# Optimization experiments

Measured on AMD Instinct MI355X. Metric: run time of the kernel, lower is better.

## Reference

```python
import jax, jax.numpy as jnp
import numpy as np
from itertools import permutations

NB_OBJ = 5
DIM_BODY = 10
DIM_OBJ = 15


def _lin(k, fi, fo):
    lim = 1.0 / np.sqrt(fi)
    k1, k2 = jax.random.split(k)
    w = jax.random.uniform(k1, (fi, fo), jnp.float32, -lim, lim)
    b = jax.random.uniform(k2, (fo,), jnp.float32, -lim, lim)
    return w, b


def setup_inputs() -> dict:
    key = jax.random.key(0)
    ks = jax.random.split(key, 12)
    B = 16384
    d = {}
    d["obs"] = jax.random.normal(ks[0], (B, DIM_BODY + NB_OBJ * DIM_OBJ), jnp.float32)
    d["act"] = jax.random.normal(ks[1], (B, 4), jnp.float32)
    d["ag"] = jax.random.uniform(ks[2], (B, 30), dtype=jnp.float32)
    d["g"] = jax.random.uniform(ks[3], (B, 30), dtype=jnp.float32)
    # GnnMessagePassing: Linear(46 -> 128), relu
    d["mp_w"], d["mp_b"] = _lin(ks[4], 46, 128)
    # PhiCriticDeepSet: two parallel 2-layer MLPs (157 -> 256 -> 256), relu
    d["phi_w1"], d["phi_b1"] = _lin(ks[5], 157, 256)
    d["phi_w2"], d["phi_b2"] = _lin(ks[6], 256, 256)
    d["phi_w3"], d["phi_b3"] = _lin(ks[7], 157, 256)
    d["phi_w4"], d["phi_b4"] = _lin(ks[8], 256, 256)
    # RhoCriticDeepSet: two Linear(256 -> 1)
    d["rho_w1"], d["rho_b1"] = _lin(ks[9], 256, 1)
    d["rho_w2"], d["rho_b2"] = _lin(ks[10], 256, 1)
    edges = np.array(list(permutations(range(NB_OBJ), 2)), np.int32)  # [20, 2]
    d["edges_src"] = jnp.array(edges[:, 0])
    d["edges_dst"] = jnp.array(edges[:, 1])
    d["pred_ids"] = jnp.array([[i, (i + 10) % 30] for i in range(20)], jnp.int32)  # [20, 2]
    inc = [[j for j in range(20) if edges[j, 1] == i] for i in range(NB_OBJ)]
    d["incoming"] = jnp.array(inc, jnp.int32)  # [5, 4]
    return d


def reference(obs, act, ag, g, mp_w, mp_b, phi_w1, phi_b1, phi_w2, phi_b2,
              phi_w3, phi_b3, phi_w4, phi_b4, rho_w1, rho_b1, rho_w2, rho_b2,
              edges_src, edges_dst, pred_ids, incoming):
    B = obs.shape[0]
    E = edges_src.shape[0]
    obs_body = obs[:, :DIM_BODY]                                   # [B, 10]
    obs_obj = obs[:, DIM_BODY:].reshape(B, NB_OBJ, DIM_OBJ)        # [B, 5, 15]
    # --- message passing over the 20 directed edges ---
    delta_g = g - ag
    dg_sel = delta_g[:, pred_ids]                                  # [B, E, 2]
    src = obs_obj[:, edges_src, :]                                 # [B, E, 15]
    dst = obs_obj[:, edges_dst, :]                                 # [B, E, 15]
    base = jnp.concatenate([obs_body, act], axis=-1)               # [B, 14]
    base_e = jnp.broadcast_to(base[:, None, :], (B, E, base.shape[-1]))
    inp_mp = jnp.concatenate([base_e, dg_sel, src, dst], axis=-1)  # [B, E, 46]
    edge_feat = jax.nn.relu(jnp.einsum('bef,fo->beo', inp_mp, mp_w) + mp_b)  # [B, E, 128]
    # --- segment-sum of incoming edges per object ---
    agg = edge_feat[:, incoming, :].sum(axis=2)                    # [B, 5, 128]
    ba = jnp.concatenate([act, obs_body], axis=-1)                 # [B, 14]
    ba_n = jnp.broadcast_to(ba[:, None, :], (B, NB_OBJ, ba.shape[-1]))
    inp = jnp.concatenate([ba_n, obs_obj, agg], axis=-1)           # [B, 5, 157]
    # --- phi deep-set critics ---
    h1 = jax.nn.relu(jnp.einsum('bnf,fh->bnh', inp, phi_w1) + phi_b1)
    o1 = jax.nn.relu(h1 @ phi_w2 + phi_b2).sum(axis=1)             # [B, 256]
    h2 = jax.nn.relu(jnp.einsum('bnf,fh->bnh', inp, phi_w3) + phi_b3)
    o2 = jax.nn.relu(h2 @ phi_w4 + phi_b4).sum(axis=1)             # [B, 256]
    # --- rho heads ---
    q1 = o1 @ rho_w1 + rho_b1                                      # [B, 1]
    q2 = o2 @ rho_w2 + rho_b2                                      # [B, 1]
    return q1, q2
```

## Files before the change

kernel.cpp:

```cpp
#include <hip/hip_runtime.h>
#include <hip/hip_bf16.h>

typedef __bf16 bf16x8 __attribute__((ext_vector_type(8)));
typedef __bf16 bf16x4 __attribute__((ext_vector_type(4)));
typedef float f32x4 __attribute__((ext_vector_type(4)));

#define MFMA(a, b, c) __builtin_amdgcn_mfma_f32_16x16x32_bf16(a, b, c, 0, 0, 0)

constexpr int MP_OFF = 0;
constexpr int W1_OFF = 8192;
constexpr int W2_OFF = 49152;
constexpr int W3_OFF = 114688;
constexpr int W4_OFF = 155648;
constexpr int WS_TOTAL = 221184;
constexpr size_t WS_BYTES = (size_t)WS_TOTAL * 2;

__device__ __forceinline__ float ldf(const void* p, int i, bool f32) {
    return f32 ? ((const float*)p)[i] : (float)(((const __bf16*)p)[i]);
}
__device__ __forceinline__ int geti(const int* p, int i, bool i64) {
    return p[i64 ? 2 * i : i];
}

__global__ void swz(const void* __restrict__ mp, const void* __restrict__ w1,
                    const void* __restrict__ w2, const void* __restrict__ w3,
                    const void* __restrict__ w4, __bf16* __restrict__ ws,
                    const unsigned short* __restrict__ uo, int* __restrict__ flags) {
    __shared__ int s_fw, s_fi;
    int tid = threadIdx.x;
    if (tid == 0) { s_fw = 0; s_fi = 0; }
    __syncthreads();
    const unsigned short* uw = (const unsigned short*)w2;
    int d = 0;
    for (int i = tid; i < 8192; i += 256)
        d |= (((uw[i] >> 7) & 0xFF) == 0xFF) ? 1 : 0;
    if (d) atomicOr(&s_fw, 1);
    if (blockIdx.x == 0) {
        int d0 = 0;
        for (int i = tid; i < 8192; i += 256)
            d0 |= (((uo[i] >> 7) & 0xFF) == 0xFF) ? 1 : 0;
        if (d0) atomicOr(&s_fi, 1);
    }
    __syncthreads();
    bool f32 = s_fw != 0;
    if (blockIdx.x == 0 && tid == 0) { flags[0] = s_fi; flags[1] = s_fw; }

    int idx = blockIdx.x * blockDim.x + tid;
    if (idx >= WS_TOTAL) return;
    const void* src;
    int base, local, nKT, nsh, style, K;
    if (idx < W1_OFF)      { src = mp; base = MP_OFF; local = idx;          nKT = 2; nsh = 7; style = 0; K = 46; }
    else if (idx < W2_OFF) { src = w1; base = W1_OFF; local = idx - W1_OFF; nKT = 5; nsh = 8; style = 1; K = 157; }
    else if (idx < W3_OFF) { src = w2; base = W2_OFF; local = idx - W2_OFF; nKT = 8; nsh = 8; style = 0; K = 256; }
    else if (idx < W4_OFF) { src = w3; base = W3_OFF; local = idx - W3_OFF; nKT = 5; nsh = 8; style = 1; K = 157; }
    else                   { src = w4; base = W4_OFF; local = idx - W4_OFF; nKT = 8; nsh = 8; style = 0; K = 256; }
    int N = 1 << nsh;
    int kp = local >> nsh, n = local & (N - 1);
    int ks = kp;
    bool ok = true;
    if (style == 1) { if (kp >= 32) ks = kp - 3; else if (kp >= 29) ok = false; }
    if (ks >= K) ok = false;
    float v = ok ? ldf(src, ks * N + n, f32) : 0.f;
    int dst = ((n >> 4) * nKT + (kp >> 5)) * 512 +
              (((((kp >> 3) & 3)) << 4) | (n & 15)) * 8 + (kp & 7);
    ws[base + dst] = (__bf16)v;
}

__device__ __forceinline__ bf16x8 gatherB(const void* W, bool f32, int style,
                                          int K, int N, int k0, int n, int q) {
    bf16x8 r;
#pragma unroll
    for (int j = 0; j < 8; ++j) {
        int k = k0 + q * 8 + j;
        bool ok = true;
        if (style == 1) { if (k >= 32) k -= 3; else if (k >= 29) ok = false; }
        if (k >= K) ok = false;
        float v = ok ? ldf(W, k * N + n, f32) : 0.f;
        r[j] = (__bf16)v;
    }
    return r;
}

template <int PC, int PBASE>
__device__ __forceinline__ void buildA(__bf16* sA, const __bf16* rb, const int* s_esrc,
                                       const int* s_pid0, const int* s_pid1, int tid) {
    for (int i = tid; i < 16 * PC * 8; i += 512) {
        int t = i >> 6, lanep = i & 63;
        int oct = ((t & 1) << 2) | (lanep >> 4);
        int r = (t >> 1) * 16 + (lanep & 15);
        int lb = r / PC, p = PBASE + r % PC;
        const __bf16* row = rb + lb * 120;
        bf16x8 v;
#pragma unroll
        for (int j = 0; j < 8; ++j) {
            int k = oct * 8 + j;
            __bf16 x = (__bf16)0.f;
            if (k < 10) x = row[k];
            else if (k < 14) x = row[85 + (k - 10)];
            else if (k < 16) x = row[89 + ((k == 14) ? s_pid0[p] : s_pid1[p])];
            else if (k < 31) x = row[10 + s_esrc[p] * 15 + (k - 16)];
            else if (k < 46) x = row[10 + (p >> 2) * 15 + (k - 31)];
            v[j] = x;
        }
        *(bf16x8*)(sA + t * 512 + lanep * 8) = v;
    }
}

template <int PC, int PBASE, bool DW>
__device__ __forceinline__ void stage1(const __bf16* Wf, const void* Wn, bool fW,
                                       const void* mp_b, const __bf16* sA,
                                       __bf16* s_inp, int wave, int lane) {
    int q = lane >> 4, c = lane & 15;
    int nt = wave;
    float mb = ldf(mp_b, nt * 16 + c, fW);
    bf16x8 bw[2];
#pragma unroll
    for (int kt = 0; kt < 2; ++kt) {
        if constexpr (DW) bw[kt] = gatherB(Wn, fW, 0, 46, 128, kt * 32, nt * 16 + c, q);
        else bw[kt] = *(const bf16x8*)(Wf + (nt * 2 + kt) * 512 + lane * 8);
    }
    f32x4 zero4 = {0.f, 0.f, 0.f, 0.f};
#pragma unroll
    for (int m = 0; m < PC; ++m) {
        f32x4 acc = zero4;
#pragma unroll
        for (int kt = 0; kt < 2; ++kt) {
            bf16x8 a = *(const bf16x8*)(sA + (m * 2 + kt) * 512 + lane * 8);
            acc = MFMA(a, bw[kt], acc);
        }
        float sum = 0.f;
#pragma unroll
        for (int rr = 0; rr < 4; ++rr) {
            float z = acc[rr] + mb;
            sum += (z > 0.f) ? z : 0.f;
        }
        int r0 = m * 16 + q * 4;
        int lb = r0 / PC;
        int o = (PBASE + r0 % PC) >> 2;
        int rinp = lb * 5 + o;
        int kk = 32 + nt * 16 + c;
        s_inp[((rinp >> 4) * 5 + (kk >> 5)) * 512 +
              ((((kk & 31) >> 3) << 4) + (rinp & 15)) * 8 + (kk & 7)] = (__bf16)sum;
    }
}

template <int MTN, bool DW>
__device__ __forceinline__ void stage2s(int mbase, const __bf16* Wf, const void* Wn,
                                        bool fW, const void* Ba, __bf16* s_h,
                                        const __bf16* s_inp, int wave, int lane) {
    int q = lane >> 4, c = lane & 15;
    f32x4 zero4 = {0.f, 0.f, 0.f, 0.f};
    f32x4 acc[2][MTN];
#pragma unroll
    for (int n = 0; n < 2; ++n)
#pragma unroll
        for (int m = 0; m < MTN; ++m) acc[n][m] = zero4;
#pragma unroll
    for (int kt = 0; kt < 5; ++kt) {
        bf16x8 b[MTN];
#pragma unroll
        for (int m = 0; m < MTN; ++m)
            b[m] = *(const bf16x8*)(s_inp + ((mbase + m) * 5 + kt) * 512 + lane * 8);
#pragma unroll
        for (int n = 0; n < 2; ++n) {
            int ht = wave * 2 + n;
            bf16x8 aw;
            if constexpr (DW) aw = gatherB(Wn, fW, 1, 157, 256, kt * 32, ht * 16 + c, q);
            else aw = *(const bf16x8*)(Wf + (ht * 5 + kt) * 512 + lane * 8);
#pragma unroll
            for (int m = 0; m < MTN; ++m) acc[n][m] = MFMA(aw, b[m], acc[n][m]);
        }
    }
    float bias_r[2][4];
#pragma unroll
    for (int n = 0; n < 2; ++n)
#pragma unroll
        for (int rg = 0; rg < 4; ++rg)
            bias_r[n][rg] = ldf(Ba, (wave * 2 + n) * 16 + q * 4 + rg, fW);
#pragma unroll
    for (int n = 0; n < 2; ++n) {
        int ht = wave * 2 + n;
#pragma unroll
        for (int m = 0; m < MTN; ++m) {
            bf16x4 hv;
#pragma unroll
            for (int rg = 0; rg < 4; ++rg) {
                float z = acc[n][m][rg] + bias_r[n][rg];
                hv[rg] = (__bf16)((z > 0.f) ? z : 0.f);
            }
            *(bf16x4*)(s_h + (m * 8 + (ht >> 1)) * 512 +
                       ((((ht & 1) * 2 + (q >> 1)) << 4) | c) * 8 + ((q & 1) << 2)) = hv;
        }
    }
}

template <int MTN, bool DW>
__device__ __forceinline__ void stage3s(int mbase, const __bf16* Wf, const void* Wn,
                                        bool fW, const void* Bb, const void* Rh,
                                        const __bf16* s_h, float* s_qp, int wave, int lane) {
    int q = lane >> 4, c = lane & 15;
    f32x4 zero4 = {0.f, 0.f, 0.f, 0.f};
    f32x4 acc[2][MTN];
#pragma unroll
    for (int n = 0; n < 2; ++n)
#pragma unroll
        for (int m = 0; m < MTN; ++m) acc[n][m] = zero4;
#pragma unroll
    for (int kt = 0; kt < 8; ++kt) {
        bf16x8 b[MTN];
#pragma unroll
        for (int m = 0; m < MTN; ++m)
            b[m] = *(const bf16x8*)(s_h + (m * 8 + kt) * 512 + lane * 8);
#pragma unroll
        for (int n = 0; n < 2; ++n) {
            int nt = wave * 2 + n;
            bf16x8 aw;
            if constexpr (DW) aw = gatherB(Wn, fW, 0, 256, 256, kt * 32, nt * 16 + c, q);
            else aw = *(const bf16x8*)(Wf + (nt * 8 + kt) * 512 + lane * 8);
#pragma unroll
            for (int m = 0; m < MTN; ++m) acc[n][m] = MFMA(aw, b[m], acc[n][m]);
        }
    }
    float bias_r[2][4], rho_r[2][4];
#pragma unroll
    for (int n = 0; n < 2; ++n)
#pragma unroll
        for (int rg = 0; rg < 4; ++rg) {
            int ncol = (wave * 2 + n) * 16 + q * 4 + rg;
            bias_r[n][rg] = ldf(Bb, ncol, fW);
            rho_r[n][rg] = ldf(Rh, ncol, fW);
        }
    float rowsum[MTN];
#pragma unroll
    for (int m = 0; m < MTN; ++m) rowsum[m] = 0.f;
#pragma unroll
    for (int n = 0; n < 2; ++n)
#pragma unroll
        for (int m = 0; m < MTN; ++m)
#pragma unroll
            for (int rg = 0; rg < 4; ++rg) {
                float z = acc[n][m][rg] + bias_r[n][rg];
                z = (z > 0.f) ? z : 0.f;
                rowsum[m] += z * rho_r[n][rg];
            }
#pragma unroll
    for (int m = 0; m < MTN; ++m) {
        float v = rowsum[m];
        v += __shfl_xor(v, 16);
        v += __shfl_xor(v, 32);
        if (q == 0) {
            int r0 = (mbase + m) * 16 + c;
            atomicAdd(&s_qp[r0 / 5], v);
        }
    }
}

template <bool DW>
__global__ __launch_bounds__(512, 6) void gn_main(
    const void* __restrict__ obs, const void* __restrict__ act,
    const void* __restrict__ ag, const void* __restrict__ g,
    const void* __restrict__ mp_b, const void* __restrict__ b1,
    const void* __restrict__ b2, const void* __restrict__ b3,
    const void* __restrict__ b4, const void* __restrict__ rw1,
    const void* __restrict__ rb1, const void* __restrict__ rw2,
    const void* __restrict__ rb2, const int* __restrict__ eA,
    const int* __restrict__ eB, const int* __restrict__ pred_ids,
    const int* __restrict__ incoming, const __bf16* __restrict__ wsW,
    const void* __restrict__ mp_w, const void* __restrict__ w1,
    const void* __restrict__ w2, const void* __restrict__ w3,
    const void* __restrict__ w4, const int* __restrict__ flags,
    float* __restrict__ out, int Btot) {
    __shared__ __align__(16) __bf16 s_union[12288];
    __shared__ __align__(16) __bf16 s_inp[12800];
    __shared__ __align__(16) float s_q[32];
    __shared__ int s_esrc[20], s_pid0[20], s_pid1[20];

    int tid = threadIdx.x, lane = tid & 63, wave = tid >> 6;
    __bf16* rb = s_union + 8192;
    int b0 = blockIdx.x * 16;

    bool fI, fW;
    if constexpr (DW) {
        const unsigned short* uo = (const unsigned short*)obs;
        const unsigned short* uw = (const unsigned short*)w2;
        int d0 = 0, d1 = 0;
        for (int i = lane; i < 8192; i += 64) {
            if (((uo[i] >> 7) & 0xFF) == 0xFF) d0 = 1;
            if (((uw[i] >> 7) & 0xFF) == 0xFF) d1 = 1;
        }
        fI = __ballot(d0) != 0;
        fW = __ballot(d1) != 0;
    } else {
        fI = flags[0] != 0;
        fW = flags[1] != 0;
    }

    bool i64_i = (incoming[1] == 0);
    bool i64_p = (pred_ids[1] == 0);
    bool i64_e = (eA[9] == 0);
    const int* es = (geti(eA, 4, i64_e) == 1) ? eA : eB;

    if (tid < 20) {
        int e = geti(incoming, tid, i64_i);
        s_esrc[tid] = geti(es, e, i64_e);
        s_pid0[tid] = geti(pred_ids, 2 * e, i64_p);
        s_pid1[tid] = geti(pred_ids, 2 * e + 1, i64_p);
    }

    for (int i = tid; i < 16 * 120; i += 512) {
        int lb = i / 120, cidx = i % 120;
        int bg = b0 + lb;
        float v = 0.f;
        if (cidx < 85) v = ldf(obs, bg * 85 + cidx, fI);
        else if (cidx < 89) v = ldf(act, bg * 4 + (cidx - 85), fI);
        else if (cidx < 119) {
            int t = cidx - 89;
            v = ldf(g, bg * 30 + t, fI) - ldf(ag, bg * 30 + t, fI);
        }
        rb[i] = (__bf16)v;
    }
    __syncthreads();

    for (int i = tid; i < 320; i += 512) {
        int mt = i >> 6, lanep = i & 63;
        int oct = lanep >> 4;
        int r = mt * 16 + (lanep & 15);
        int lb = r / 5, o = r % 5;
        const __bf16* row = rb + lb * 120;
        bf16x8 v;
#pragma unroll
        for (int j = 0; j < 8; ++j) {
            int k = oct * 8 + j;
            __bf16 x = (__bf16)0.f;
            if (k < 4) x = row[85 + k];
            else if (k < 14) x = row[k - 4];
            else if (k < 29) x = row[10 + o * 15 + (k - 14)];
            v[j] = x;
        }
        *(bf16x8*)(s_inp + mt * 2560 + lanep * 8) = v;
    }
    buildA<8, 0>(s_union, rb, s_esrc, s_pid0, s_pid1, tid);
    __syncthreads();
    stage1<8, 0, DW>(wsW + MP_OFF, mp_w, fW, mp_b, s_union, s_inp, wave, lane);
    __syncthreads();
    buildA<8, 8>(s_union, rb, s_esrc, s_pid0, s_pid1, tid);
    __syncthreads();
    stage1<8, 8, DW>(wsW + MP_OFF, mp_w, fW, mp_b, s_union, s_inp, wave, lane);
    __syncthreads();
    buildA<4, 16>(s_union, rb, s_esrc, s_pid0, s_pid1, tid);
    __syncthreads();
    stage1<4, 16, DW>(wsW + MP_OFF, mp_w, fW, mp_b, s_union, s_inp, wave, lane);
    if (tid < 32) s_q[tid] = 0.f;
    __syncthreads();

    for (int P = 0; P < 2; ++P) {
        const __bf16* Wa = wsW + (P ? W3_OFF : W1_OFF);
        const __bf16* Wb = wsW + (P ? W4_OFF : W2_OFF);
        const void* Wan = P ? w3 : w1;
        const void* Wbn = P ? w4 : w2;
        const void* ba = P ? b3 : b1;
        const void* bb = P ? b4 : b2;
        const void* rho = P ? rw2 : rw1;
        float* qp = s_q + P * 16;
        stage2s<3, DW>(0, Wa, Wan, fW, ba, s_union, s_inp, wave, lane);
        __syncthreads();
        stage3s<3, DW>(0, Wb, Wbn, fW, bb, rho, s_union, qp, wave, lane);
        __syncthreads();
        stage2s<2, DW>(3, Wa, Wan, fW, ba, s_union, s_inp, wave, lane);
        __syncthreads();
        stage3s<2, DW>(3, Wb, Wbn, fW, bb, rho, s_union, qp, wave, lane);
        __syncthreads();
    }

    if (tid < 16) {
        out[b0 + tid] = s_q[tid] + ldf(rb1, 0, fW);
        out[Btot + b0 + tid] = s_q[16 + tid] + ldf(rb2, 0, fW);
    }
}

extern "C" void kernel_launch(void* const* d_in, const int* in_sizes, int n_in,
                              void* d_out, int out_size, void* d_ws, size_t ws_size,
                              hipStream_t stream) {
    int B = out_size / 2;

    const void *obs = nullptr, *act = nullptr, *ag = nullptr, *g = nullptr;
    const void *mp_w = nullptr, *mp_b = nullptr;
    const void *w1 = nullptr, *b1 = nullptr, *w2 = nullptr, *b2 = nullptr;
    const void *w3 = nullptr, *b3 = nullptr, *w4 = nullptr, *b4 = nullptr;
    const void *rw1 = nullptr, *rb1 = nullptr, *rw2 = nullptr, *rb2 = nullptr;
    const int *eA = nullptr, *eB = nullptr, *pred = nullptr, *inc = nullptr;
    int c30 = 0, c256 = 0, c1 = 0, c40k = 0, c65k = 0, c20 = 0;
    for (int i = 0; i < n_in; ++i) {
        int sz = in_sizes[i];
        const void* p = d_in[i];
        if (sz == B * 85) obs = p;
        else if (sz == B * 30) { if (c30++ == 0) ag = p; else g = p; }
        else if (sz == 5888) mp_w = p;
        else if (sz == 128) mp_b = p;
        else if (sz == 40192) { if (c40k++ == 0) w1 = p; else w3 = p; }
        else if (sz == 65536 || sz == B * 4) {
            int c = c65k++;
            if (c == 0) act = p; else if (c == 1) w2 = p; else w4 = p;
        }
        else if (sz == 256) {
            int c = c256++;
            if (c == 0) b1 = p; else if (c == 1) b2 = p; else if (c == 2) b3 = p;
            else if (c == 3) b4 = p; else if (c == 4) rw1 = p; else rw2 = p;
        }
        else if (sz == 1) { if (c1++ == 0) rb1 = p; else rb2 = p; }
        else if (sz == 40) pred = (const int*)p;
        else if (sz == 20) {
            int c = c20++;
            if (c == 0) eA = (const int*)p;
            else if (c == 1) eB = (const int*)p;
            else inc = (const int*)p;
        }
    }
    if (!obs || !act || !ag || !g || !mp_w || !mp_b || !w1 || !b1 || !w2 || !b2 ||
        !w3 || !b3 || !w4 || !b4 || !rw1 || !rb1 || !rw2 || !rb2 || !eA || !eB ||
        !pred || !inc) {
        obs = d_in[0]; act = d_in[1]; ag = d_in[2]; g = d_in[3];
        mp_w = d_in[4]; mp_b = d_in[5]; w1 = d_in[6]; b1 = d_in[7];
        w2 = d_in[8]; b2 = d_in[9]; w3 = d_in[10]; b3 = d_in[11];
        w4 = d_in[12]; b4 = d_in[13]; rw1 = d_in[14]; rb1 = d_in[15];
        rw2 = d_in[16]; rb2 = d_in[17];
        eA = (const int*)d_in[18]; eB = (const int*)d_in[19];
        pred = (const int*)d_in[20]; inc = (const int*)d_in[21];
    }

    float* out = (float*)d_out;
    __bf16* wsW = (__bf16*)d_ws;
    bool use_ws = ws_size >= WS_BYTES + 8;
    int* flags = (int*)((char*)d_ws + WS_BYTES);
    int grid = B / 16;

    if (use_ws) {
        swz<<<(WS_TOTAL + 255) / 256, 256, 0, stream>>>(
            mp_w, w1, w2, w3, w4, wsW, (const unsigned short*)obs, flags);
        gn_main<false><<<grid, 512, 0, stream>>>(
            obs, act, ag, g, mp_b, b1, b2, b3, b4, rw1, rb1, rw2, rb2,
            eA, eB, pred, inc, wsW, mp_w, w1, w2, w3, w4, flags, out, B);
    } else {
        gn_main<true><<<grid, 512, 0, stream>>>(
            obs, act, ag, g, mp_b, b1, b2, b3, b4, rw1, rb1, rw2, rb2,
            eA, eB, pred, inc, wsW, mp_w, w1, w2, w3, w4, flags, out, B);
    }
}
```

Baseline: 178.7 us.

## Move per-block input staging buffer from LDS to global workspace to raise occupancy

Moves the 25.6KB per-block input tile (s_inp) out of LDS into a per-block slice of the global workspace when the workspace is large enough. The reduction buffer rb becomes its own small LDS array. The aim is to cut LDS use per block so more blocks can be resident, and launch bounds go up to 8 blocks per CU. The cost is that the staged inputs are now read and written through global memory/L2 instead of LDS, with higher latency, and the higher occupancy target may force register spills.

```diff
diff --git a/kernel.cpp b/kernel.cpp
--- a/kernel.cpp
+++ b/kernel.cpp
@@ -14,6 +14,8 @@
 constexpr int W4_OFF = 155648;
 constexpr int WS_TOTAL = 221184;
 constexpr size_t WS_BYTES = (size_t)WS_TOTAL * 2;
+constexpr size_t GINP_OFF = WS_BYTES + 64;
+constexpr int INP_ELEMS = 12800;
 
 __device__ __forceinline__ float ldf(const void* p, int i, bool f32) {
     return f32 ? ((const float*)p)[i] : (float)(((const __bf16*)p)[i]);
@@ -255,8 +257,8 @@
     }
 }
 
-template <bool DW>
-__global__ __launch_bounds__(512, 6) void gn_main(
+template <bool DW, bool GINP>
+__global__ __launch_bounds__(512, GINP ? 8 : 6) void gn_main(
     const void* __restrict__ obs, const void* __restrict__ act,
     const void* __restrict__ ag, const void* __restrict__ g,
     const void* __restrict__ mp_b, const void* __restrict__ b1,
@@ -269,15 +271,16 @@
     const void* __restrict__ mp_w, const void* __restrict__ w1,
     const void* __restrict__ w2, const void* __restrict__ w3,
     const void* __restrict__ w4, const int* __restrict__ flags,
-    float* __restrict__ out, int Btot) {
+    __bf16* __restrict__ ginp_base, float* __restrict__ out, int Btot) {
     __shared__ __align__(16) __bf16 s_union[12288];
-    __shared__ __align__(16) __bf16 s_inp[12800];
+    __shared__ __align__(16) __bf16 rb[1920];
+    __shared__ __align__(16) __bf16 s_inp_lds[GINP ? 8 : 12800];
     __shared__ __align__(16) float s_q[32];
     __shared__ int s_esrc[20], s_pid0[20], s_pid1[20];
 
     int tid = threadIdx.x, lane = tid & 63, wave = tid >> 6;
-    __bf16* rb = s_union + 8192;
     int b0 = blockIdx.x * 16;
+    __bf16* s_inp = GINP ? (ginp_base + (size_t)blockIdx.x * INP_ELEMS) : s_inp_lds;
 
     bool fI, fW;
     if constexpr (DW) {
@@ -430,19 +433,28 @@
 
     float* out = (float*)d_out;
     __bf16* wsW = (__bf16*)d_ws;
+    int grid = B / 16;
+    size_t ginp_bytes = (size_t)grid * INP_ELEMS * 2;
     bool use_ws = ws_size >= WS_BYTES + 8;
+    bool use_ginp = ws_size >= GINP_OFF + ginp_bytes;
     int* flags = (int*)((char*)d_ws + WS_BYTES);
-    int grid = B / 16;
+    __bf16* ginp = (__bf16*)((char*)d_ws + GINP_OFF);
 
     if (use_ws) {
         swz<<<(WS_TOTAL + 255) / 256, 256, 0, stream>>>(
             mp_w, w1, w2, w3, w4, wsW, (const unsigned short*)obs, flags);
-        gn_main<false><<<grid, 512, 0, stream>>>(
+        if (use_ginp) {
+            gn_main<false, true><<<grid, 512, 0, stream>>>(
+                obs, act, ag, g, mp_b, b1, b2, b3, b4, rw1, rb1, rw2, rb2,
+                eA, eB, pred, inc, wsW, mp_w, w1, w2, w3, w4, flags, ginp, out, B);
+        } else {
+            gn_main<false, false><<<grid, 512, 0, stream>>>(
+                obs, act, ag, g, mp_b, b1, b2, b3, b4, rw1, rb1, rw2, rb2,
+                eA, eB, pred, inc, wsW, mp_w, w1, w2, w3, w4, flags, ginp, out, B);
+        }
+    } else {
+        gn_main<true, false><<<grid, 512, 0, stream>>>(
             obs, act, ag, g, mp_b, b1, b2, b3, b4, rw1, rb1, rw2, rb2,
-            eA, eB, pred, inc, wsW, mp_w, w1, w2, w3, w4, flags, out, B);
-    } else {
-        gn_main<true><<<grid, 512, 0, stream>>>(
-            obs, act, ag, g, mp_b, b1, b2, b3, b4, rw1, rb1, rw2, rb2,
-            eA, eB, pred, inc, wsW, mp_w, w1, w2, w3, w4, flags, out, B);
-    }
-}
+            eA, eB, pred, inc, wsW, mp_w, w1, w2, w3, w4, flags, ginp, out, B);
+    }
+}
```

Result: slower. 226.6 us (+26.8%).

## Shrink LDS footprint to raise occupancy by recomputing first K-tile from raw rows

Applied to the files above, without the earlier changes.

Drops the stored first K-tile (body/object features) of the phi input and rebuilds it on the fly from the raw row buffer inside stage2s. The edge stage and the phi stages are split into smaller chunks so the scratch union buffer shrinks. Together these cut LDS per block enough to request 8 blocks per CU instead of 6. The cost is more barriers and smaller MFMA batches per pass, plus scattered LDS reads to rebuild the first tile.

```diff
diff --git a/kernel.cpp b/kernel.cpp
--- a/kernel.cpp
+++ b/kernel.cpp
@@ -139,7 +139,7 @@
         int o = (PBASE + r0 % PC) >> 2;
         int rinp = lb * 5 + o;
         int kk = 32 + nt * 16 + c;
-        s_inp[((rinp >> 4) * 5 + (kk >> 5)) * 512 +
+        s_inp[((rinp >> 4) * 4 + (kk >> 5) - 1) * 512 +
               ((((kk & 31) >> 3) << 4) + (rinp & 15)) * 8 + (kk & 7)] = (__bf16)sum;
     }
 }
@@ -147,7 +147,8 @@
 template <int MTN, bool DW>
 __device__ __forceinline__ void stage2s(int mbase, const __bf16* Wf, const void* Wn,
                                         bool fW, const void* Ba, __bf16* s_h,
-                                        const __bf16* s_inp, int wave, int lane) {
+                                        const __bf16* s_inp, const __bf16* rb,
+                                        int wave, int lane) {
     int q = lane >> 4, c = lane & 15;
     f32x4 zero4 = {0.f, 0.f, 0.f, 0.f};
     f32x4 acc[2][MTN];
@@ -158,9 +159,29 @@
 #pragma unroll
     for (int kt = 0; kt < 5; ++kt) {
         bf16x8 b[MTN];
-#pragma unroll
-        for (int m = 0; m < MTN; ++m)
-            b[m] = *(const bf16x8*)(s_inp + ((mbase + m) * 5 + kt) * 512 + lane * 8);
+        if (kt == 0) {
+#pragma unroll
+            for (int m = 0; m < MTN; ++m) {
+                int rinp = (mbase + m) * 16 + c;
+                int lb = rinp / 5, o = rinp - lb * 5;
+                const __bf16* row = rb + lb * 120;
+                bf16x8 v;
+#pragma unroll
+                for (int j = 0; j < 8; ++j) {
+                    int k = q * 8 + j;
+                    __bf16 x = (__bf16)0.f;
+                    if (k < 4) x = row[85 + k];
+                    else if (k < 14) x = row[k - 4];
+                    else if (k < 29) x = row[10 + o * 15 + (k - 14)];
+                    v[j] = x;
+                }
+                b[m] = v;
+            }
+        } else {
+#pragma unroll
+            for (int m = 0; m < MTN; ++m)
+                b[m] = *(const bf16x8*)(s_inp + ((mbase + m) * 4 + kt - 1) * 512 + lane * 8);
+        }
 #pragma unroll
         for (int n = 0; n < 2; ++n) {
             int ht = wave * 2 + n;
@@ -256,7 +277,7 @@
 }
 
 template <bool DW>
-__global__ __launch_bounds__(512, 6) void gn_main(
+__global__ __launch_bounds__(512, 8) void gn_main(
     const void* __restrict__ obs, const void* __restrict__ act,
     const void* __restrict__ ag, const void* __restrict__ g,
     const void* __restrict__ mp_b, const void* __restrict__ b1,
@@ -270,14 +291,16 @@
     const void* __restrict__ w2, const void* __restrict__ w3,
     const void* __restrict__ w4, const int* __restrict__ flags,
     float* __restrict__ out, int Btot) {
-    __shared__ __align__(16) __bf16 s_union[12288];
-    __shared__ __align__(16) __bf16 s_inp[12800];
+    __shared__ __align__(16) __bf16 s_union[8192];
+    __shared__ __align__(16) __bf16 rb[1920];
+    __shared__ __align__(16) __bf16 s_inp[10240];
     __shared__ __align__(16) float s_q[32];
-    __shared__ int s_esrc[20], s_pid0[20], s_pid1[20];
 
     int tid = threadIdx.x, lane = tid & 63, wave = tid >> 6;
-    __bf16* rb = s_union + 8192;
     int b0 = blockIdx.x * 16;
+    int* s_esrc = (int*)(s_union + 4096);
+    int* s_pid0 = s_esrc + 20;
+    int* s_pid1 = s_esrc + 40;
 
     bool fI, fW;
     if constexpr (DW) {
@@ -321,31 +344,21 @@
     }
     __syncthreads();
 
-    for (int i = tid; i < 320; i += 512) {
-        int mt = i >> 6, lanep = i & 63;
-        int oct = lanep >> 4;
-        int r = mt * 16 + (lanep & 15);
-        int lb = r / 5, o = r % 5;
-        const __bf16* row = rb + lb * 120;
-        bf16x8 v;
-#pragma unroll
-        for (int j = 0; j < 8; ++j) {
-            int k = oct * 8 + j;
-            __bf16 x = (__bf16)0.f;
-            if (k < 4) x = row[85 + k];
-            else if (k < 14) x = row[k - 4];
-            else if (k < 29) x = row[10 + o * 15 + (k - 14)];
-            v[j] = x;
-        }
-        *(bf16x8*)(s_inp + mt * 2560 + lanep * 8) = v;
-    }
-    buildA<8, 0>(s_union, rb, s_esrc, s_pid0, s_pid1, tid);
-    __syncthreads();
-    stage1<8, 0, DW>(wsW + MP_OFF, mp_w, fW, mp_b, s_union, s_inp, wave, lane);
-    __syncthreads();
-    buildA<8, 8>(s_union, rb, s_esrc, s_pid0, s_pid1, tid);
-    __syncthreads();
-    stage1<8, 8, DW>(wsW + MP_OFF, mp_w, fW, mp_b, s_union, s_inp, wave, lane);
+    buildA<4, 0>(s_union, rb, s_esrc, s_pid0, s_pid1, tid);
+    __syncthreads();
+    stage1<4, 0, DW>(wsW + MP_OFF, mp_w, fW, mp_b, s_union, s_inp, wave, lane);
+    __syncthreads();
+    buildA<4, 4>(s_union, rb, s_esrc, s_pid0, s_pid1, tid);
+    __syncthreads();
+    stage1<4, 4, DW>(wsW + MP_OFF, mp_w, fW, mp_b, s_union, s_inp, wave, lane);
+    __syncthreads();
+    buildA<4, 8>(s_union, rb, s_esrc, s_pid0, s_pid1, tid);
+    __syncthreads();
+    stage1<4, 8, DW>(wsW + MP_OFF, mp_w, fW, mp_b, s_union, s_inp, wave, lane);
+    __syncthreads();
+    buildA<4, 12>(s_union, rb, s_esrc, s_pid0, s_pid1, tid);
+    __syncthreads();
+    stage1<4, 12, DW>(wsW + MP_OFF, mp_w, fW, mp_b, s_union, s_inp, wave, lane);
     __syncthreads();
     buildA<4, 16>(s_union, rb, s_esrc, s_pid0, s_pid1, tid);
     __syncthreads();
@@ -362,13 +375,17 @@
         const void* bb = P ? b4 : b2;
         const void* rho = P ? rw2 : rw1;
         float* qp = s_q + P * 16;
-        stage2s<3, DW>(0, Wa, Wan, fW, ba, s_union, s_inp, wave, lane);
-        __syncthreads();
-        stage3s<3, DW>(0, Wb, Wbn, fW, bb, rho, s_union, qp, wave, lane);
-        __syncthreads();
-        stage2s<2, DW>(3, Wa, Wan, fW, ba, s_union, s_inp, wave, lane);
-        __syncthreads();
-        stage3s<2, DW>(3, Wb, Wbn, fW, bb, rho, s_union, qp, wave, lane);
+        stage2s<2, DW>(0, Wa, Wan, fW, ba, s_union, s_inp, rb, wave, lane);
+        __syncthreads();
+        stage3s<2, DW>(0, Wb, Wbn, fW, bb, rho, s_union, qp, wave, lane);
+        __syncthreads();
+        stage2s<2, DW>(2, Wa, Wan, fW, ba, s_union, s_inp, rb, wave, lane);
+        __syncthreads();
+        stage3s<2, DW>(2, Wb, Wbn, fW, bb, rho, s_union, qp, wave, lane);
+        __syncthreads();
+        stage2s<1, DW>(4, Wa, Wan, fW, ba, s_union, s_inp, rb, wave, lane);
+        __syncthreads();
+        stage3s<1, DW>(4, Wb, Wbn, fW, bb, rho, s_union, qp, wave, lane);
         __syncthreads();
     }
 
```

Result: slower. 263.1 us (+47.2%).
